# Performance work log

Measured on AMD Instinct MI355X. Metric: run time of the kernel, lower is better.

Reference implementation:

```python
import jax, jax.numpy as jnp
import numpy as np

T, B = 256, 512
IMG_FLAT = 25          # 5*5*num_channels
FEAT = 16; LOC = 4; EMB = 4
LSTM_IN = FEAT + LOC + EMB  # 24
H = 128
GRID = 10.0


def _lin(k, out_d, in_d, scale=0.05):
    kw, kb = jax.random.split(k)
    return (jax.random.normal(kw, (out_d, in_d), jnp.float32) * scale,
            jax.random.normal(kb, (out_d,), jnp.float32) * scale)


def setup_inputs() -> dict:
    key = jax.random.key(0)
    ks = jax.random.split(key, 16)
    image = jax.random.uniform(ks[0], (T * B, 5, 5), jnp.float32) * 255.0
    location = jax.random.uniform(ks[1], (T * B, 2), jnp.float32) * GRID
    message = jax.random.normal(ks[2], (T * B, 1), jnp.float32)
    done = jax.random.randint(ks[3], (T * B,), 0, 2, jnp.int32)
    h0 = jnp.zeros((1, B, H), jnp.float32)
    c0 = jnp.zeros((1, B, H), jnp.float32)
    Wv1, bv1 = _lin(ks[4], 256, IMG_FLAT)
    Wv2, bv2 = _lin(ks[5], 256, 256)
    Wv3, bv3 = _lin(ks[6], 128, 256)
    Wv4, bv4 = _lin(ks[7], FEAT, 128)
    Wl, bl = _lin(ks[8], LOC, 2)
    Wm, bm = _lin(ks[9], EMB, 1)
    Wih, bih = _lin(ks[10], 4 * H, LSTM_IN)
    Whh, bhh = _lin(ks[11], 4 * H, H)
    return dict(image=image, location=location, message=message, done=done,
                h0=h0, c0=c0,
                Wv1=Wv1, bv1=bv1, Wv2=Wv2, bv2=bv2, Wv3=Wv3, bv3=bv3,
                Wv4=Wv4, bv4=bv4, Wl=Wl, bl=bl, Wm=Wm, bm=bm,
                Wih=Wih, bih=bih, Whh=Whh, bhh=bhh)


def _get_states(image, location, message, done_f, h0, c0,
                Wv1, bv1, Wv2, bv2, Wv3, bv3, Wv4, bv4,
                Wl, bl, Wm, bm, Wih, bih, Whh, bhh):
    batch = h0.shape[1]
    # encoders (all rows at once, faithful to torch version)
    x = image.reshape(image.shape[0], -1) / 255.0
    f = jax.nn.relu(x @ Wv1.T + bv1)
    f = jax.nn.relu(f @ Wv2.T + bv2)
    f = jax.nn.relu(f @ Wv3.T + bv3)
    image_feat = jax.nn.relu(f @ Wv4.T + bv4)                  # [TB, 16]
    loc_feat = (location / GRID) @ Wl.T + bl                    # [TB, 4]
    msg = (1.0 - done_f)[:, None] * message
    msg_feat = jax.nn.relu(msg @ Wm.T + bm)                     # [TB, 4]
    hid = jnp.concatenate([image_feat, loc_feat, msg_feat], axis=1)
    hid = hid.reshape(-1, batch, LSTM_IN)                       # [T, B, 24]
    d_seq = done_f.reshape(-1, batch)                           # [T, B]

    def step(carry, xd):
        h, c = carry
        x_t, d_t = xd
        mask = (1.0 - d_t)[:, None]
        h = h * mask
        c = c * mask
        gates = x_t @ Wih.T + bih + h @ Whh.T + bhh             # [B, 4H]
        i, fg, g, o = jnp.split(gates, 4, axis=-1)
        c = jax.nn.sigmoid(fg) * c + jax.nn.sigmoid(i) * jnp.tanh(g)
        h = jax.nn.sigmoid(o) * jnp.tanh(c)
        return (h, c), h

    (hT, cT), hs = jax.lax.scan(step, (h0[0], c0[0]), (hid, d_seq))
    new_hidden = hs.reshape(-1, H)                              # [TB, 128]
    return new_hidden, hT[None], cT[None]


def reference(image, location, message, done, h0, c0,
              Wv1, bv1, Wv2, bv2, Wv3, bv3, Wv4, bv4,
              Wl, bl, Wm, bm, Wih, bih, Whh, bhh):
    done_f = done.astype(jnp.float32)
    return _get_states(image, location, message, done_f, h0, c0,
                       Wv1, bv1, Wv2, bv2, Wv3, bv3, Wv4, bv4,
                       Wl, bl, Wm, bm, Wih, bih, Whh, bhh)
```

## Files before the change

### kernel.cpp

```cpp
#include <hip/hip_runtime.h>
#include <hip/hip_bf16.h>

#define T_STEPS 256
#define BATCH   512
#define HID     128
#define TBROWS  (T_STEPS * BATCH)
#define XH_STRIDE 32

typedef short  bh8   __attribute__((ext_vector_type(8)));
typedef _Float16 h8  __attribute__((ext_vector_type(8)));
typedef float  f32x4 __attribute__((ext_vector_type(4)));

__device__ __forceinline__ unsigned short f2bf_bits(float x) {
    union { float f; unsigned int u; } a; a.f = x;
    unsigned int r = a.u + 0x7fffu + ((a.u >> 16) & 1u);
    return (unsigned short)(r >> 16);
}
__device__ __forceinline__ unsigned short f2h_bits(float x) {
    union { _Float16 h; unsigned short u; } z; z.h = (_Float16)x; return z.u;
}
__device__ __forceinline__ unsigned int pack2h(float a, float b) {
    union { _Float16 h[2]; unsigned int u; } z;
    z.h[0] = (_Float16)a; z.h[1] = (_Float16)b; return z.u;
}
__device__ __forceinline__ unsigned int pack2bf(float a, float b) {
    return (unsigned int)f2bf_bits(a) | ((unsigned int)f2bf_bits(b) << 16);
}

#if __has_builtin(__builtin_amdgcn_rcpf)
__device__ __forceinline__ float frcp(float x) { return __builtin_amdgcn_rcpf(x); }
#else
__device__ __forceinline__ float frcp(float x) { return 1.0f / x; }
#endif
#if __has_builtin(__builtin_amdgcn_exp2f)
__device__ __forceinline__ float fexp2(float x) { return __builtin_amdgcn_exp2f(x); }
#else
__device__ __forceinline__ float fexp2(float x) { return __expf(x * 0.6931471806f); }
#endif
#define LOG2E 1.442695041f
__device__ __forceinline__ float sigf(float x) {
    return frcp(1.0f + fexp2(-x * LOG2E));
}
__device__ __forceinline__ float tanh_fast(float x) {
    return fmaf(-2.0f, frcp(1.0f + fexp2(x * (2.0f * LOG2E))), 1.0f);
}

__device__ __forceinline__ void fragstore(unsigned short* dst, const float* W,
                                          int i, int NT, int Kreal) {
    const int j    = i & 7;
    const int lane = (i >> 3) & 63;
    const int ts   = i >> 9;
    const int nt   = ts % NT;
    const int ks   = ts / NT;
    const int n = nt * 16 + (lane & 15);
    const int k = ks * 32 + (lane >> 4) * 8 + j;
    dst[i] = (k < Kreal) ? f2bf_bits(W[n * Kreal + k]) : (unsigned short)0;
}

#define NE1 8192
#define NE2 65536
#define NE3 32768
#define NE4 2048
#define NWC 81920
#define NBS 512
#define PREP_TOTAL (NE1 + NE2 + NE3 + NE4 + NWC + NBS)

__global__ __launch_bounds__(256) void prep_kernel(
    const float* __restrict__ W1, const float* __restrict__ W2,
    const float* __restrict__ W3, const float* __restrict__ W4,
    const float* __restrict__ Wih, const float* __restrict__ bih,
    const float* __restrict__ Whh, const float* __restrict__ bhh,
    unsigned short* __restrict__ w1f, unsigned short* __restrict__ w2f,
    unsigned short* __restrict__ w3f, unsigned short* __restrict__ w4f,
    unsigned short* __restrict__ wcf, float* __restrict__ bsum)
{
    int i = blockIdx.x * 256 + threadIdx.x;
    if (i < NE1) { fragstore(w1f, W1, i, 16, 25); return; }
    i -= NE1;
    if (i < NE2) { fragstore(w2f, W2, i, 16, 256); return; }
    i -= NE2;
    if (i < NE3) { fragstore(w3f, W3, i, 8, 256); return; }
    i -= NE3;
    if (i < NE4) { fragstore(w4f, W4, i, 1, 128); return; }
    i -= NE4;
    if (i < NWC) {
        const int j    = i & 7;
        const int lane = (i >> 3) & 63;
        const int ts   = i >> 9;
        const int mt   = ts / 5;
        const int kt   = ts - mt * 5;
        const int m = mt * 16 + (lane & 15);
        const int k = kt * 32 + (lane >> 4) * 8 + j;
        float v = 0.0f;
        if (k < 128)      v = Whh[m * 128 + k];
        else if (k < 152) v = Wih[m * 24 + (k - 128)];
        wcf[i] = f2h_bits(v);
        return;
    }
    i -= NWC;
    if (i < NBS) bsum[i] = bih[i] + bhh[i];
}

#define ASTRIDE 264

__global__ __launch_bounds__(256) void encoder_kernel(
    const float* __restrict__ img,
    const float* __restrict__ loc,
    const float* __restrict__ msg,
    const int*   __restrict__ done,
    const float* __restrict__ B1, const float* __restrict__ B2,
    const float* __restrict__ B3, const float* __restrict__ B4,
    const float* __restrict__ Wl, const float* __restrict__ Bl,
    const float* __restrict__ Wm, const float* __restrict__ Bm,
    const unsigned short* __restrict__ w1f, const unsigned short* __restrict__ w2f,
    const unsigned short* __restrict__ w3f, const unsigned short* __restrict__ w4f,
    unsigned short* __restrict__ xcat_h)
{
    __shared__ __align__(16) unsigned short actA[4][32][ASTRIDE];
    __shared__ __align__(16) unsigned short actB[4][32][ASTRIDE];

    const int tid  = threadIdx.x;
    const int w    = tid >> 6;
    const int lane = tid & 63;
    const int n    = lane & 15;
    const int quad = lane >> 4;
    const int wrow0 = blockIdx.x * 128 + w * 32;

    if (tid < 128) {
        const int grow = blockIdx.x * 128 + tid;
        const float l0 = loc[(size_t)grow * 2 + 0] * 0.1f;
        const float l1 = loc[(size_t)grow * 2 + 1] * 0.1f;
        #pragma unroll
        for (int c = 0; c < 4; ++c)
            xcat_h[(size_t)grow * XH_STRIDE + 16 + c] =
                f2h_bits(fmaf(Wl[c * 2 + 0], l0, fmaf(Wl[c * 2 + 1], l1, Bl[c])));
        const float mm = (1.0f - (float)done[grow]) * msg[grow];
        #pragma unroll
        for (int c = 0; c < 4; ++c)
            xcat_h[(size_t)grow * XH_STRIDE + 20 + c] =
                f2h_bits(fmaxf(fmaf(Wm[c], mm, Bm[c]), 0.0f));
    }

    const f32x4 zero4 = {0.0f, 0.0f, 0.0f, 0.0f};

    {
        bh8 bimg[2];
        #pragma unroll
        for (int sg = 0; sg < 2; ++sg) {
            const size_t grow = wrow0 + sg * 16 + n;
            #pragma unroll
            for (int j = 0; j < 8; ++j) {
                const int k = quad * 8 + j;
                const float v = (k < 25) ? img[grow * 25 + k] * (1.0f / 255.0f) : 0.0f;
                bimg[sg][j] = (short)f2bf_bits(v);
            }
        }
        f32x4 a1[16][2];
        #pragma unroll
        for (int mt = 0; mt < 16; ++mt) {
            const bh8 a = *reinterpret_cast<const bh8*>(w1f + (size_t)(mt * 64 + lane) * 8);
            a1[mt][0] = __builtin_amdgcn_mfma_f32_16x16x32_bf16(a, bimg[0], zero4, 0, 0, 0);
            a1[mt][1] = __builtin_amdgcn_mfma_f32_16x16x32_bf16(a, bimg[1], zero4, 0, 0, 0);
        }
        #pragma unroll
        for (int mt = 0; mt < 16; ++mt) {
            const float4 bv = *reinterpret_cast<const float4*>(B1 + mt * 16 + quad * 4);
            #pragma unroll
            for (int sg = 0; sg < 2; ++sg) {
                const float v0 = fmaxf(a1[mt][sg][0] + bv.x, 0.0f);
                const float v1 = fmaxf(a1[mt][sg][1] + bv.y, 0.0f);
                const float v2 = fmaxf(a1[mt][sg][2] + bv.z, 0.0f);
                const float v3 = fmaxf(a1[mt][sg][3] + bv.w, 0.0f);
                uint2 pk; pk.x = pack2bf(v0, v1); pk.y = pack2bf(v2, v3);
                *reinterpret_cast<uint2*>(&actA[w][sg * 16 + n][mt * 16 + quad * 4]) = pk;
            }
        }
    }
    __syncthreads();

    {
        f32x4 a2[16][2];
        #pragma unroll
        for (int mt = 0; mt < 16; ++mt) { a2[mt][0] = zero4; a2[mt][1] = zero4; }
        #pragma unroll
        for (int kt = 0; kt < 8; ++kt) {
            const bh8 b0 = *reinterpret_cast<const bh8*>(&actA[w][n][kt * 32 + quad * 8]);
            const bh8 b1 = *reinterpret_cast<const bh8*>(&actA[w][16 + n][kt * 32 + quad * 8]);
            #pragma unroll
            for (int mt = 0; mt < 16; ++mt) {
                const bh8 a = *reinterpret_cast<const bh8*>(
                    w2f + (size_t)((kt * 16 + mt) * 64 + lane) * 8);
                a2[mt][0] = __builtin_amdgcn_mfma_f32_16x16x32_bf16(a, b0, a2[mt][0], 0, 0, 0);
                a2[mt][1] = __builtin_amdgcn_mfma_f32_16x16x32_bf16(a, b1, a2[mt][1], 0, 0, 0);
            }
        }
        #pragma unroll
        for (int mt = 0; mt < 16; ++mt) {
            const float4 bv = *reinterpret_cast<const float4*>(B2 + mt * 16 + quad * 4);
            #pragma unroll
            for (int sg = 0; sg < 2; ++sg) {
                const float v0 = fmaxf(a2[mt][sg][0] + bv.x, 0.0f);
                const float v1 = fmaxf(a2[mt][sg][1] + bv.y, 0.0f);
                const float v2 = fmaxf(a2[mt][sg][2] + bv.z, 0.0f);
                const float v3 = fmaxf(a2[mt][sg][3] + bv.w, 0.0f);
                uint2 pk; pk.x = pack2bf(v0, v1); pk.y = pack2bf(v2, v3);
                *reinterpret_cast<uint2*>(&actB[w][sg * 16 + n][mt * 16 + quad * 4]) = pk;
            }
        }
    }
    __syncthreads();

    {
        f32x4 a3[8][2];
        #pragma unroll
        for (int mt = 0; mt < 8; ++mt) { a3[mt][0] = zero4; a3[mt][1] = zero4; }
        #pragma unroll
        for (int kt = 0; kt < 8; ++kt) {
            const bh8 b0 = *reinterpret_cast<const bh8*>(&actB[w][n][kt * 32 + quad * 8]);
            const bh8 b1 = *reinterpret_cast<const bh8*>(&actB[w][16 + n][kt * 32 + quad * 8]);
            #pragma unroll
            for (int mt = 0; mt < 8; ++mt) {
                const bh8 a = *reinterpret_cast<const bh8*>(
                    w3f + (size_t)((kt * 8 + mt) * 64 + lane) * 8);
                a3[mt][0] = __builtin_amdgcn_mfma_f32_16x16x32_bf16(a, b0, a3[mt][0], 0, 0, 0);
                a3[mt][1] = __builtin_amdgcn_mfma_f32_16x16x32_bf16(a, b1, a3[mt][1], 0, 0, 0);
            }
        }
        #pragma unroll
        for (int mt = 0; mt < 8; ++mt) {
            const float4 bv = *reinterpret_cast<const float4*>(B3 + mt * 16 + quad * 4);
            #pragma unroll
            for (int sg = 0; sg < 2; ++sg) {
                const float v0 = fmaxf(a3[mt][sg][0] + bv.x, 0.0f);
                const float v1 = fmaxf(a3[mt][sg][1] + bv.y, 0.0f);
                const float v2 = fmaxf(a3[mt][sg][2] + bv.z, 0.0f);
                const float v3 = fmaxf(a3[mt][sg][3] + bv.w, 0.0f);
                uint2 pk; pk.x = pack2bf(v0, v1); pk.y = pack2bf(v2, v3);
                *reinterpret_cast<uint2*>(&actA[w][sg * 16 + n][mt * 16 + quad * 4]) = pk;
            }
        }
    }
    __syncthreads();

    {
        f32x4 a4[2] = {zero4, zero4};
        #pragma unroll
        for (int kt = 0; kt < 4; ++kt) {
            const bh8 b0 = *reinterpret_cast<const bh8*>(&actA[w][n][kt * 32 + quad * 8]);
            const bh8 b1 = *reinterpret_cast<const bh8*>(&actA[w][16 + n][kt * 32 + quad * 8]);
            const bh8 a = *reinterpret_cast<const bh8*>(w4f + (size_t)(kt * 64 + lane) * 8);
            a4[0] = __builtin_amdgcn_mfma_f32_16x16x32_bf16(a, b0, a4[0], 0, 0, 0);
            a4[1] = __builtin_amdgcn_mfma_f32_16x16x32_bf16(a, b1, a4[1], 0, 0, 0);
        }
        const float4 bv = *reinterpret_cast<const float4*>(B4 + quad * 4);
        #pragma unroll
        for (int sg = 0; sg < 2; ++sg) {
            const int grow = wrow0 + sg * 16 + n;
            const float v0 = fmaxf(a4[sg][0] + bv.x, 0.0f);
            const float v1 = fmaxf(a4[sg][1] + bv.y, 0.0f);
            const float v2 = fmaxf(a4[sg][2] + bv.z, 0.0f);
            const float v3 = fmaxf(a4[sg][3] + bv.w, 0.0f);
            uint2 pk; pk.x = pack2h(v0, v1); pk.y = pack2h(v2, v3);
            *reinterpret_cast<uint2*>(xcat_h + (size_t)grow * XH_STRIDE + quad * 4) = pk;
        }
    }
}

#define COLS 2
#define HXS 168

__global__ __launch_bounds__(256) void lstm_kernel(
    const unsigned short* __restrict__ xcat_h,
    const int*   __restrict__ done,
    const float* __restrict__ h0,
    const float* __restrict__ c0,
    const unsigned short* __restrict__ wcf,
    const float* __restrict__ bsum,
    float* __restrict__ out)
{
    __shared__ __align__(16) unsigned short hx[2][16][HXS];
    __shared__ __align__(16) float gbuf[COLS][130][4];

    const int tid  = threadIdx.x;
    const int w    = tid >> 6;
    const int lane = tid & 63;
    const int n    = lane & 15;
    const int quad = lane >> 4;
    const int bb   = blockIdx.x * COLS;

    h8 wf[2][4][5];
    #pragma unroll
    for (int h = 0; h < 2; ++h)
        #pragma unroll
        for (int g = 0; g < 4; ++g)
            #pragma unroll
            for (int kt = 0; kt < 5; ++kt)
                wf[h][g][kt] = *reinterpret_cast<const h8*>(
                    wcf + (size_t)(((g * 8 + w + 4 * h) * 5 + kt) * 64 + lane) * 8);

    const int tn = tid >> 7;
    const int tu = tid & 127;
    float bi_t[4];
    #pragma unroll
    for (int g = 0; g < 4; ++g) bi_t[g] = bsum[g * 128 + tu];

    float c_ = c0[(size_t)(bb + tn) * HID + tu];
    const float h0v = h0[(size_t)(bb + tn) * HID + tu];

    for (int i = tid; i < 2 * 16 * HXS / 2; i += 256)
        reinterpret_cast<unsigned int*>(hx)[i] = 0u;
    __syncthreads();

    int mc = done[bb + tn];
    int mn = done[BATCH + bb + tn];
    hx[0][tn][tu] = f2h_bits(h0v * (1.0f - (float)mc));
    if (tid < COLS * 12) {
        const int nl = tid / 12, kp = tid - nl * 12;
        *reinterpret_cast<unsigned int*>(&hx[0][nl][128 + 2 * kp]) =
            *reinterpret_cast<const unsigned int*>(
                xcat_h + (size_t)(bb + nl) * XH_STRIDE + 2 * kp);
    }
    __syncthreads();

    float hl = 0.0f;

    #pragma unroll 1
    for (int s = 0; s < T_STEPS; ++s) {
        const int buf = s & 1;

        h8 bf[5];
        #pragma unroll
        for (int kt = 0; kt < 5; ++kt)
            bf[kt] = *reinterpret_cast<const h8*>(&hx[buf][n][kt * 32 + quad * 8]);

        unsigned int xreg = 0;
        if (tid < COLS * 12) {
            const int nl = tid / 12, kp = tid - nl * 12;
            const int rowx = (s + 1 < T_STEPS ? s + 1 : T_STEPS - 1) * BATCH + bb + nl;
            xreg = *reinterpret_cast<const unsigned int*>(
                xcat_h + (size_t)rowx * XH_STRIDE + 2 * kp);
        }
        const int mf = done[(s + 2 < T_STEPS ? s + 2 : T_STEPS - 1) * BATCH + bb + tn];

        f32x4 acc[2][4];
        #pragma unroll
        for (int h = 0; h < 2; ++h)
            #pragma unroll
            for (int g = 0; g < 4; ++g) acc[h][g] = (f32x4){0.0f, 0.0f, 0.0f, 0.0f};
        #pragma unroll
        for (int kt = 0; kt < 5; ++kt)
            #pragma unroll
            for (int h = 0; h < 2; ++h)
                #pragma unroll
                for (int g = 0; g < 4; ++g)
                    acc[h][g] = __builtin_amdgcn_mfma_f32_16x16x32_f16(
                        wf[h][g][kt], bf[kt], acc[h][g], 0, 0, 0);

        if (n < COLS) {
            #pragma unroll
            for (int h = 0; h < 2; ++h) {
                const int ub = (w + 4 * h) * 16 + quad * 4;
                #pragma unroll
                for (int r = 0; r < 4; ++r) {
                    float4 gv;
                    gv.x = acc[h][0][r]; gv.y = acc[h][1][r];
                    gv.z = acc[h][2][r]; gv.w = acc[h][3][r];
                    *reinterpret_cast<float4*>(&gbuf[n][ub + r][0]) = gv;
                }
            }
        }
        __syncthreads();

        const float4 gv = *reinterpret_cast<const float4*>(&gbuf[tn][tu][0]);
        const float mcur = 1.0f - (float)mc;
        const float mnxt = 1.0f - (float)mn;
        const float gi = gv.x + bi_t[0];
        const float gf = gv.y + bi_t[1];
        const float gg = gv.z + bi_t[2];
        const float go = gv.w + bi_t[3];
        const float cn = sigf(gf) * (c_ * mcur) + sigf(gi) * tanh_fast(gg);
        const float hn = sigf(go) * tanh_fast(cn);
        c_ = cn; hl = hn;

        const int row = s * BATCH + bb + tn;
        out[(size_t)row * HID + tu] = hn;
        hx[buf ^ 1][tn][tu] = f2h_bits(hn * mnxt);
        if (tid < COLS * 12) {
            const int nl = tid / 12, kp = tid - nl * 12;
            *reinterpret_cast<unsigned int*>(&hx[buf ^ 1][nl][128 + 2 * kp]) = xreg;
        }
        mc = mn; mn = mf;
        __syncthreads();
    }

    const size_t base = (size_t)TBROWS * HID;
    out[base + (size_t)(bb + tn) * HID + tu] = hl;
    out[base + (size_t)BATCH * HID + (size_t)(bb + tn) * HID + tu] = c_;
}

extern "C" void kernel_launch(void* const* d_in, const int* in_sizes, int n_in,
                              void* d_out, int out_size, void* d_ws, size_t ws_size,
                              hipStream_t stream) {
    const float* img  = (const float*)d_in[0];
    const float* loc  = (const float*)d_in[1];
    const float* msg  = (const float*)d_in[2];
    const int*   done = (const int*)d_in[3];
    const float* h0   = (const float*)d_in[4];
    const float* c0   = (const float*)d_in[5];
    const float* W1   = (const float*)d_in[6];
    const float* B1   = (const float*)d_in[7];
    const float* W2   = (const float*)d_in[8];
    const float* B2   = (const float*)d_in[9];
    const float* W3   = (const float*)d_in[10];
    const float* B3   = (const float*)d_in[11];
    const float* W4   = (const float*)d_in[12];
    const float* B4   = (const float*)d_in[13];
    const float* Wl   = (const float*)d_in[14];
    const float* Bl   = (const float*)d_in[15];
    const float* Wm   = (const float*)d_in[16];
    const float* Bm   = (const float*)d_in[17];
    const float* Wih  = (const float*)d_in[18];
    const float* bih  = (const float*)d_in[19];
    const float* Whh  = (const float*)d_in[20];
    const float* bhh  = (const float*)d_in[21];

    char* wsb = (char*)d_ws;
    unsigned short* xcat_h = (unsigned short*)wsb;
    unsigned short* w1f = (unsigned short*)(wsb + (size_t)TBROWS * XH_STRIDE * 2);
    unsigned short* w2f = w1f + NE1;
    unsigned short* w3f = w2f + NE2;
    unsigned short* w4f = w3f + NE3;
    unsigned short* wcf = w4f + NE4;
    float*          bsum = (float*)(wcf + NWC);

    float* out = (float*)d_out;

    prep_kernel<<<(PREP_TOTAL + 255) / 256, 256, 0, stream>>>(
        W1, W2, W3, W4, Wih, bih, Whh, bhh,
        w1f, w2f, w3f, w4f, wcf, bsum);
    encoder_kernel<<<TBROWS / 128, 256, 0, stream>>>(
        img, loc, msg, done, B1, B2, B3, B4, Wl, Bl, Wm, Bm,
        w1f, w2f, w3f, w4f, xcat_h);
    lstm_kernel<<<BATCH / COLS, 256, 0, stream>>>(
        xcat_h, done, h0, c0, wcf, bsum, out);
}
```

Baseline: 402.8 us.

## Run LSTM with one batch column per block and batch hidden-state stores

```diff
diff --git a/kernel.cpp b/kernel.cpp
--- a/kernel.cpp
+++ b/kernel.cpp
@@ -103,7 +103,7 @@
 
 #define ASTRIDE 264
 
-__global__ __launch_bounds__(256) void encoder_kernel(
+__global__ __launch_bounds__(256, 2) void encoder_kernel(
     const float* __restrict__ img,
     const float* __restrict__ loc,
     const float* __restrict__ msg,
@@ -266,10 +266,9 @@
     }
 }
 
-#define COLS 2
 #define HXS 168
 
-__global__ __launch_bounds__(256) void lstm_kernel(
+__global__ __launch_bounds__(256, 2) void lstm_kernel(
     const unsigned short* __restrict__ xcat_h,
     const int*   __restrict__ done,
     const float* __restrict__ h0,
@@ -279,14 +278,15 @@
     float* __restrict__ out)
 {
     __shared__ __align__(16) unsigned short hx[2][16][HXS];
-    __shared__ __align__(16) float gbuf[COLS][130][4];
+    __shared__ __align__(16) float gbuf[130][4];
+    __shared__ __align__(16) float hist[8][HID];
 
     const int tid  = threadIdx.x;
     const int w    = tid >> 6;
     const int lane = tid & 63;
     const int n    = lane & 15;
     const int quad = lane >> 4;
-    const int bb   = blockIdx.x * COLS;
+    const int b    = blockIdx.x;
 
     h8 wf[2][4][5];
     #pragma unroll
@@ -298,33 +298,30 @@
                 wf[h][g][kt] = *reinterpret_cast<const h8*>(
                     wcf + (size_t)(((g * 8 + w + 4 * h) * 5 + kt) * 64 + lane) * 8);
 
-    const int tn = tid >> 7;
     const int tu = tid & 127;
     float bi_t[4];
     #pragma unroll
     for (int g = 0; g < 4; ++g) bi_t[g] = bsum[g * 128 + tu];
 
-    float c_ = c0[(size_t)(bb + tn) * HID + tu];
-    const float h0v = h0[(size_t)(bb + tn) * HID + tu];
-
-    for (int i = tid; i < 2 * 16 * HXS / 2; i += 256)
+    float c_ = 0.0f, hl = 0.0f;
+    if (tid < 128) c_ = c0[(size_t)b * HID + tu];
+
+    for (int i = tid; i < (int)(sizeof(hx) / 4); i += 256)
         reinterpret_cast<unsigned int*>(hx)[i] = 0u;
     __syncthreads();
 
-    int mc = done[bb + tn];
-    int mn = done[BATCH + bb + tn];
-    hx[0][tn][tu] = f2h_bits(h0v * (1.0f - (float)mc));
-    if (tid < COLS * 12) {
-        const int nl = tid / 12, kp = tid - nl * 12;
-        *reinterpret_cast<unsigned int*>(&hx[0][nl][128 + 2 * kp]) =
-            *reinterpret_cast<const unsigned int*>(
-                xcat_h + (size_t)(bb + nl) * XH_STRIDE + 2 * kp);
-    }
+    int mc = done[b];
+    int mn = done[BATCH + b];
+    if (tid < 128) {
+        const float h0v = h0[(size_t)b * HID + tu];
+        hx[0][0][tu] = f2h_bits(h0v * (1.0f - (float)mc));
+    }
+    if (tid < 12)
+        reinterpret_cast<unsigned int*>(&hx[0][0][128])[tid] =
+            reinterpret_cast<const unsigned int*>(xcat_h + (size_t)b * XH_STRIDE)[tid];
     __syncthreads();
 
-    float hl = 0.0f;
-
-    #pragma unroll 1
+    #pragma unroll 2
     for (int s = 0; s < T_STEPS; ++s) {
         const int buf = s & 1;
 
@@ -334,13 +331,11 @@
             bf[kt] = *reinterpret_cast<const h8*>(&hx[buf][n][kt * 32 + quad * 8]);
 
         unsigned int xreg = 0;
-        if (tid < COLS * 12) {
-            const int nl = tid / 12, kp = tid - nl * 12;
-            const int rowx = (s + 1 < T_STEPS ? s + 1 : T_STEPS - 1) * BATCH + bb + nl;
-            xreg = *reinterpret_cast<const unsigned int*>(
-                xcat_h + (size_t)rowx * XH_STRIDE + 2 * kp);
-        }
-        const int mf = done[(s + 2 < T_STEPS ? s + 2 : T_STEPS - 1) * BATCH + bb + tn];
+        if (tid < 12) {
+            const int rowx = (s + 1 < T_STEPS ? s + 1 : T_STEPS - 1) * BATCH + b;
+            xreg = reinterpret_cast<const unsigned int*>(xcat_h + (size_t)rowx * XH_STRIDE)[tid];
+        }
+        const int mf = done[(s + 2 < T_STEPS ? s + 2 : T_STEPS - 1) * BATCH + b];
 
         f32x4 acc[2][4];
         #pragma unroll
@@ -356,7 +351,7 @@
                     acc[h][g] = __builtin_amdgcn_mfma_f32_16x16x32_f16(
                         wf[h][g][kt], bf[kt], acc[h][g], 0, 0, 0);
 
-        if (n < COLS) {
+        if (n == 0) {
             #pragma unroll
             for (int h = 0; h < 2; ++h) {
                 const int ub = (w + 4 * h) * 16 + quad * 4;
@@ -365,37 +360,45 @@
                     float4 gv;
                     gv.x = acc[h][0][r]; gv.y = acc[h][1][r];
                     gv.z = acc[h][2][r]; gv.w = acc[h][3][r];
-                    *reinterpret_cast<float4*>(&gbuf[n][ub + r][0]) = gv;
+                    *reinterpret_cast<float4*>(&gbuf[ub + r][0]) = gv;
                 }
             }
         }
         __syncthreads();
 
-        const float4 gv = *reinterpret_cast<const float4*>(&gbuf[tn][tu][0]);
-        const float mcur = 1.0f - (float)mc;
-        const float mnxt = 1.0f - (float)mn;
-        const float gi = gv.x + bi_t[0];
-        const float gf = gv.y + bi_t[1];
-        const float gg = gv.z + bi_t[2];
-        const float go = gv.w + bi_t[3];
-        const float cn = sigf(gf) * (c_ * mcur) + sigf(gi) * tanh_fast(gg);
-        const float hn = sigf(go) * tanh_fast(cn);
-        c_ = cn; hl = hn;
-
-        const int row = s * BATCH + bb + tn;
-        out[(size_t)row * HID + tu] = hn;
-        hx[buf ^ 1][tn][tu] = f2h_bits(hn * mnxt);
-        if (tid < COLS * 12) {
-            const int nl = tid / 12, kp = tid - nl * 12;
-            *reinterpret_cast<unsigned int*>(&hx[buf ^ 1][nl][128 + 2 * kp]) = xreg;
-        }
+        if (tid < 128) {
+            const float4 gv = *reinterpret_cast<const float4*>(&gbuf[tu][0]);
+            const float mcur = 1.0f - (float)mc;
+            const float mnxt = 1.0f - (float)mn;
+            const float gi = gv.x + bi_t[0];
+            const float gf = gv.y + bi_t[1];
+            const float gg = gv.z + bi_t[2];
+            const float go = gv.w + bi_t[3];
+            const float cn = sigf(gf) * (c_ * mcur) + sigf(gi) * tanh_fast(gg);
+            const float hn = sigf(go) * tanh_fast(cn);
+            c_ = cn; hl = hn;
+            hist[s & 7][tu] = hn;
+            hx[buf ^ 1][0][tu] = f2h_bits(hn * mnxt);
+        }
+        if (tid < 12)
+            reinterpret_cast<unsigned int*>(&hx[buf ^ 1][0][128])[tid] = xreg;
         mc = mn; mn = mf;
         __syncthreads();
-    }
-
-    const size_t base = (size_t)TBROWS * HID;
-    out[base + (size_t)(bb + tn) * HID + tu] = hl;
-    out[base + (size_t)BATCH * HID + (size_t)(bb + tn) * HID + tu] = c_;
+
+        if ((s & 7) == 7) {
+            const int sc = tid >> 5;
+            const int j  = tid & 31;
+            const float4 v = *reinterpret_cast<const float4*>(&hist[sc][j * 4]);
+            const int srow = (s - 7 + sc) * BATCH + b;
+            *reinterpret_cast<float4*>(out + (size_t)srow * HID + j * 4) = v;
+        }
+    }
+
+    if (tid < 128) {
+        const size_t base = (size_t)TBROWS * HID;
+        out[base + (size_t)b * HID + tu] = hl;
+        out[base + (size_t)BATCH * HID + (size_t)b * HID + tu] = c_;
+    }
 }
 
 extern "C" void kernel_launch(void* const* d_in, const int* in_sizes, int n_in,
@@ -441,6 +444,6 @@
     encoder_kernel<<<TBROWS / 128, 256, 0, stream>>>(
         img, loc, msg, done, B1, B2, B3, B4, Wl, Bl, Wm, Bm,
         w1f, w2f, w3f, w4f, xcat_h);
-    lstm_kernel<<<BATCH / COLS, 256, 0, stream>>>(
+    lstm_kernel<<<BATCH, 256, 0, stream>>>(
         xcat_h, done, h0, c0, wcf, bsum, out);
 }
```

Result: slower. 507.5 us (+26.0%).
